# Performance work log

Measured on AMD Instinct MI355X. Metric: run time of the kernel, lower is better.

## Reference

```python
import jax, jax.numpy as jnp
import numpy as np

B, L, D, V = 512, 128, 512, 100000

def setup_inputs() -> dict:
    key = jax.random.key(0)
    ks = jax.random.split(key, 8)
    return {
        "t1s": jax.random.randint(ks[0], (B,), 0, V),
        "t2s": jax.random.randint(ks[1], (B,), 0, V),
        "t1_contexts": jax.random.randint(ks[2], (B, L), 0, V),
        "t2_contexts": jax.random.randint(ks[3], (B, L), 0, V),
        "embed_table": jax.random.normal(ks[4], (V, D), dtype=jnp.float32),
        "att_mat": jax.random.normal(ks[5], (D, D), dtype=jnp.float32) * (6.0 / (D + D)) ** 0.5,
        "w_pred": jax.random.normal(ks[6], (D, 1), dtype=jnp.float32) * 0.02,
        "b_pred": jnp.zeros((1,), dtype=jnp.float32),
    }

def _frob_normalize(x):
    # torch.norm(mat, p=2) is the Frobenius norm of the whole (L, D) matrix
    n = jnp.sqrt(jnp.sum(x * x, axis=(1, 2), keepdims=True))
    return x / n

def reference(t1s, t2s, t1_contexts, t2_contexts, embed_table, att_mat, w_pred, b_pred):
    # dropout is identity in eval mode; t1s/t2s embeddings are unused in the
    # 'dynamic' branch (dead code in the original forward).
    A = _frob_normalize(embed_table[t1_contexts])  # (B, L, D)
    Bm = _frob_normalize(embed_table[t2_contexts])  # (B, L, D)
    # batched bilinear attention: tanh(A @ att_mat @ B^T)
    S = jnp.tanh(jnp.einsum('bld,de,bme->blm', A, att_mat, Bm))  # (B, L, L)
    rows = jax.nn.softmax(jnp.mean(S, axis=2), axis=1)  # (B, L)
    cols = jax.nn.softmax(jnp.mean(S, axis=1), axis=1)  # (B, L)
    newA = jnp.einsum('bld,bl->bd', A, rows)   # (B, D)
    newB = jnp.einsum('bld,bl->bd', Bm, cols)  # (B, D)
    logits = ((newA * newB) @ w_pred + b_pred).reshape(-1)  # (B,)
    return logits, S
```

## Files before the change

### kernel.cpp

```cpp
#include <hip/hip_runtime.h>
#include <hip/hip_bf16.h>
#include <stdint.h>

#define NB 512
#define NL 128
#define ND 512

typedef __bf16 bf16;
typedef __bf16 bf16x8 __attribute__((ext_vector_type(8)));
typedef float  f32x4  __attribute__((ext_vector_type(4)));

#define GLDS(src, dst) __builtin_amdgcn_global_load_lds( \
    (const __attribute__((address_space(1))) void*)(src), \
    (__attribute__((address_space(3))) void*)(dst), 16, 0, 0)

__global__ __launch_bounds__(256) void k_gather(const int* __restrict__ ctx1,
                                                const int* __restrict__ ctx2,
                                                const float* __restrict__ table,
                                                bf16* __restrict__ d1,
                                                bf16* __restrict__ d2,
                                                float* __restrict__ ss,
                                                const float* __restrict__ att,
                                                bf16* __restrict__ attT) {
    const int b = blockIdx.x, side = blockIdx.y, zc = blockIdx.z, t = threadIdx.x;
    if (side == 2) {
        int chunk = b * 8 + zc;
        if (chunk < 1024) {
            int i = chunk * 256 + t;
            int n = i >> 9, k = i & 511;
            attT[i] = (bf16)att[k * 512 + n];
        }
        return;
    }
    const int* __restrict__ ctx = side ? ctx2 : ctx1;
    bf16* __restrict__ dst = side ? d2 : d1;
    const int base = b * NL;
    const int dv = t & 127, lr = t >> 7;
    int idxs[8];
    #pragma unroll
    for (int i = 0; i < 8; ++i) idxs[i] = ctx[base + zc * 16 + i * 2 + lr];
    float acc = 0.f;
    #pragma unroll
    for (int i = 0; i < 8; ++i) {
        int l = zc * 16 + i * 2 + lr;
        f32x4 v = __builtin_nontemporal_load(
            (const f32x4*)table + (size_t)idxs[i] * (ND / 4) + dv);
        acc += v[0]*v[0] + v[1]*v[1] + v[2]*v[2] + v[3]*v[3];
        union { bf16 h[4]; uint2 u; } pk;
        pk.h[0] = (bf16)v[0]; pk.h[1] = (bf16)v[1];
        pk.h[2] = (bf16)v[2]; pk.h[3] = (bf16)v[3];
        *((uint2*)(dst + (size_t)(base + l) * ND) + dv) = pk.u;
    }
    for (int o = 32; o; o >>= 1) acc += __shfl_xor(acc, o);
    __shared__ float red[4];
    if ((t & 63) == 0) red[t >> 6] = acc;
    __syncthreads();
    if (t == 0) atomicAdd(&ss[side * NB + b], red[0] + red[1] + red[2] + red[3]);
}

__global__ __launch_bounds__(512) void k_mega2(
        const bf16* __restrict__ Ab, const bf16* __restrict__ attT,
        const bf16* __restrict__ Bb, float* __restrict__ Sout,
        const float* __restrict__ ss, const float* __restrict__ w_pred,
        const float* __restrict__ b_pred, float* __restrict__ logits) {
    const int b = blockIdx.x, row0 = b * NL, tid = threadIdx.x;
    const int lane = tid & 63, w = tid >> 6;
    const int lm = lane & 15, quad = lane >> 4;
    const int wm  = (w & 1) * 64;
    const int wn1 = (w >> 1) * 128;
    const int wn2 = (w >> 1) * 32;

    __shared__ __align__(16) char smem[163840];
    bf16* stA0 = (bf16*)smem;
    bf16* stA1 = (bf16*)(smem + 8192);
    bf16* stT0 = (bf16*)(smem + 16384);
    bf16* stT1 = (bf16*)(smem + 49152);
    bf16* Tls  = (bf16*)smem;
    bf16* sB0  = (bf16*)(smem + 131072);
    bf16* sB1  = (bf16*)(smem + 139264);
    bf16* sC0  = (bf16*)(smem + 147456);
    bf16* sC1  = (bf16*)(smem + 155648);
    float* rowb = (float*)smem;
    float* colb = (float*)(smem + 2048);
    float* wrow = (float*)(smem + 3072);
    float* wcol = (float*)(smem + 3584);
    float* red2 = (float*)(smem + 4096);

    const float ssA = ss[b], ssB = ss[NB + b];

    #define STAGE1(k0, dA, dT) do {                                          \
        { int r_ = tid >> 2, sl_ = tid & 3, cs_ = sl_ ^ ((r_ >> 1) & 3);     \
          GLDS(Ab + (size_t)(row0 + r_) * ND + (k0) + cs_ * 8, (dA) + tid * 8); } \
        _Pragma("unroll")                                                    \
        for (int i_ = 0; i_ < 4; ++i_) {                                     \
            int s_ = i_ * 512 + tid, r_ = s_ >> 2, sl_ = s_ & 3;             \
            int cs_ = sl_ ^ ((r_ >> 1) & 3);                                 \
            GLDS(attT + (size_t)r_ * ND + (k0) + cs_ * 8, (dT) + s_ * 8); }  \
    } while (0)
    #define STAGE2(k0, dB, dC) do {                                          \
        int r_ = tid >> 2, sl_ = tid & 3, cs_ = sl_ ^ ((r_ >> 1) & 3);       \
        GLDS(Bb + (size_t)(row0 + r_) * ND + (k0) + cs_ * 8, (dB) + tid * 8);\
        GLDS(Ab + (size_t)(row0 + r_) * ND + (k0) + cs_ * 8, (dC) + tid * 8);\
    } while (0)

    f32x4 acc1[4][8] = {};
    STAGE1(0, stA0, stT0);

    for (int t = 0; t < 16; ++t) {
        if (t < 15) {
            STAGE1((t + 1) * 32, (t & 1) ? stA0 : stA1, (t & 1) ? stT0 : stT1);
            asm volatile("s_waitcnt vmcnt(5)" ::: "memory");
        } else {
            STAGE2(0, sB0, sC0);
            asm volatile("s_waitcnt vmcnt(2)" ::: "memory");
        }
        __builtin_amdgcn_s_barrier();
        const bf16* A_ = (t & 1) ? stA1 : stA0;
        const bf16* T_ = (t & 1) ? stT1 : stT0;
        bf16x8 af[4], bfm[8];
        #pragma unroll
        for (int t4 = 0; t4 < 4; ++t4) {
            int R = wm + t4 * 16 + lm;
            af[t4] = *(const bf16x8*)&A_[R * 32 + (quad ^ ((R >> 1) & 3)) * 8];
        }
        #pragma unroll
        for (int t8 = 0; t8 < 8; ++t8) {
            int R = wn1 + t8 * 16 + lm;
            bfm[t8] = *(const bf16x8*)&T_[R * 32 + (quad ^ ((R >> 1) & 3)) * 8];
        }
        __builtin_amdgcn_s_setprio(1);
        #pragma unroll
        for (int im = 0; im < 4; ++im)
            #pragma unroll
            for (int jn = 0; jn < 8; ++jn)
                acc1[im][jn] = __builtin_amdgcn_mfma_f32_16x16x32_bf16(
                    af[im], bfm[jn], acc1[im][jn], 0, 0, 0);
        __builtin_amdgcn_s_setprio(0);
        __builtin_amdgcn_s_barrier();
    }

    #pragma unroll
    for (int im = 0; im < 4; ++im)
    #pragma unroll
    for (int jn = 0; jn < 8; ++jn)
    #pragma unroll
    for (int p = 0; p < 4; ++p) {
        int m = wm + im * 16 + quad * 4 + p;
        int n = wn1 + jn * 16 + lm;
        int ks = n >> 5, kq = (n >> 3) & 3, e = n & 7;
        int pos = kq ^ ((m >> 2) & 3);
        Tls[ks * 4096 + m * 32 + pos * 8 + e] = (bf16)acc1[im][jn][p];
    }
    __syncthreads();

    f32x4 acc2[4][2] = {}, accG[4][2] = {};

    for (int t = 0; t < 16; ++t) {
        if (t < 15) {
            STAGE2((t + 1) * 32, (t & 1) ? sB0 : sB1, (t & 1) ? sC0 : sC1);
            asm volatile("s_waitcnt vmcnt(2)" ::: "memory");
        } else {
            asm volatile("s_waitcnt vmcnt(0)" ::: "memory");
        }
        __builtin_amdgcn_s_barrier();
        const bf16* B_ = (t & 1) ? sB1 : sB0;
        const bf16* C_ = (t & 1) ? sC1 : sC0;
        float4 w0 = *(const float4*)(w_pred + t * 32 + quad * 8);
        float4 w1 = *(const float4*)(w_pred + t * 32 + quad * 8 + 4);
        float wv[8] = {w0.x, w0.y, w0.z, w0.w, w1.x, w1.y, w1.z, w1.w};
        bf16x8 af[4], af2[4], bf2[2], bfw[2];
        #pragma unroll
        for (int t4 = 0; t4 < 4; ++t4) {
            int R = wm + t4 * 16 + lm;
            af[t4]  = *(const bf16x8*)&Tls[t * 4096 + R * 32 + (quad ^ ((R >> 2) & 3)) * 8];
            af2[t4] = *(const bf16x8*)&C_[R * 32 + (quad ^ ((R >> 1) & 3)) * 8];
        }
        #pragma unroll
        for (int t2 = 0; t2 < 2; ++t2) {
            int R = wn2 + t2 * 16 + lm;
            bf2[t2] = *(const bf16x8*)&B_[R * 32 + (quad ^ ((R >> 1) & 3)) * 8];
            #pragma unroll
            for (int j = 0; j < 8; ++j)
                bfw[t2][j] = (bf16)((float)bf2[t2][j] * wv[j]);
        }
        __builtin_amdgcn_s_setprio(1);
        #pragma unroll
        for (int im = 0; im < 4; ++im)
            #pragma unroll
            for (int jn = 0; jn < 2; ++jn) {
                acc2[im][jn] = __builtin_amdgcn_mfma_f32_16x16x32_bf16(
                    af[im], bf2[jn], acc2[im][jn], 0, 0, 0);
                accG[im][jn] = __builtin_amdgcn_mfma_f32_16x16x32_bf16(
                    af2[im], bfw[jn], accG[im][jn], 0, 0, 0);
            }
        __builtin_amdgcn_s_setprio(0);
        __builtin_amdgcn_s_barrier();
    }

    const float sc = rsqrtf(ssA * ssB);
    float* __restrict__ Sb = Sout + (size_t)b * NL * NL;
    #pragma unroll
    for (int im = 0; im < 4; ++im)
    #pragma unroll
    for (int jn = 0; jn < 2; ++jn)
    #pragma unroll
    for (int p = 0; p < 4; ++p) {
        float v = tanhf(acc2[im][jn][p] * sc);
        acc2[im][jn][p] = v;
        int m = wm + im * 16 + quad * 4 + p;
        int n = wn2 + jn * 16 + lm;
        __builtin_nontemporal_store(v, &Sb[m * NL + n]);
    }
    #pragma unroll
    for (int im = 0; im < 4; ++im)
    #pragma unroll
    for (int p = 0; p < 4; ++p) {
        float r = acc2[im][0][p] + acc2[im][1][p];
        r += __shfl_xor(r, 1); r += __shfl_xor(r, 2);
        r += __shfl_xor(r, 4); r += __shfl_xor(r, 8);
        if (lm == 0) rowb[(w >> 1) * NL + wm + im * 16 + quad * 4 + p] = r;
    }
    #pragma unroll
    for (int jn = 0; jn < 2; ++jn) {
        float cv = 0.f;
        #pragma unroll
        for (int im = 0; im < 4; ++im)
            #pragma unroll
            for (int p = 0; p < 4; ++p) cv += acc2[im][jn][p];
        cv += __shfl_xor(cv, 16); cv += __shfl_xor(cv, 32);
        if (quad == 0) colb[(w & 1) * NL + wn2 + jn * 16 + lm] = cv;
    }
    __syncthreads();

    if (tid < 64) {
        float a  = (rowb[tid] + rowb[NL + tid] + rowb[2 * NL + tid] + rowb[3 * NL + tid]) * (1.f / NL);
        float c2 = (rowb[tid + 64] + rowb[NL + tid + 64] + rowb[2 * NL + tid + 64] + rowb[3 * NL + tid + 64]) * (1.f / NL);
        float mx = fmaxf(a, c2);
        for (int o = 32; o; o >>= 1) mx = fmaxf(mx, __shfl_xor(mx, o));
        float e0 = expf(a - mx), e1 = expf(c2 - mx);
        float s = e0 + e1;
        for (int o = 32; o; o >>= 1) s += __shfl_xor(s, o);
        float inv = 1.f / s;
        wrow[tid] = e0 * inv; wrow[tid + 64] = e1 * inv;
    } else if (tid < 128) {
        int q = tid - 64;
        float a  = (colb[q] + colb[NL + q]) * (1.f / NL);
        float c2 = (colb[q + 64] + colb[NL + q + 64]) * (1.f / NL);
        float mx = fmaxf(a, c2);
        for (int o = 32; o; o >>= 1) mx = fmaxf(mx, __shfl_xor(mx, o));
        float e0 = expf(a - mx), e1 = expf(c2 - mx);
        float s = e0 + e1;
        for (int o = 32; o; o >>= 1) s += __shfl_xor(s, o);
        float inv = 1.f / s;
        wcol[q] = e0 * inv; wcol[q + 64] = e1 * inv;
    }
    __syncthreads();

    float wc0 = wcol[wn2 + lm], wc1 = wcol[wn2 + 16 + lm];
    float g = 0.f;
    #pragma unroll
    for (int im = 0; im < 4; ++im)
    #pragma unroll
    for (int p = 0; p < 4; ++p) {
        float wr = wrow[wm + im * 16 + quad * 4 + p];
        g += wr * (wc0 * accG[im][0][p] + wc1 * accG[im][1][p]);
    }
    for (int o = 32; o; o >>= 1) g += __shfl_xor(g, o);
    if (lane == 0) red2[w] = g;
    __syncthreads();
    if (tid == 0) {
        float tot = 0.f;
        #pragma unroll
        for (int i = 0; i < 8; ++i) tot += red2[i];
        logits[b] = tot * sc + b_pred[0];
    }
}

extern "C" void kernel_launch(void* const* d_in, const int* in_sizes, int n_in,
                              void* d_out, int out_size, void* d_ws, size_t ws_size,
                              hipStream_t stream) {
    const int*   t1c = (const int*)d_in[2];
    const int*   t2c = (const int*)d_in[3];
    const float* emb = (const float*)d_in[4];
    const float* att = (const float*)d_in[5];
    const float* wp  = (const float*)d_in[6];
    const float* bp  = (const float*)d_in[7];

    float* out    = (float*)d_out;
    float* logits = out;
    float* S      = out + NB;

    char* ws = (char*)d_ws;
    bf16*  Ab   = (bf16*)(ws);
    bf16*  Bb   = (bf16*)(ws + 67108864);
    bf16*  attT = (bf16*)(ws + 134217728);
    float* ss   = (float*)(ws + 134742016);

    hipMemsetAsync(ss, 0, 4096, stream);
    k_gather<<<dim3(NB, 3, 8), 256, 0, stream>>>(t1c, t2c, emb, Ab, Bb, ss, att, attT);
    k_mega2<<<dim3(NB), 512, 0, stream>>>(Ab, attT, Bb, S, ss, wp, bp, logits);
}
```

Baseline: 398.5 us.

## Move B-side embedding gather into main kernel, overlapped with first GEMM

The second context's embedding gather and sum-of-squares no longer run in the separate gather kernel. They move into the main kernel, where each iteration of the first GEMM loop issues row loads two steps ahead and commits them to the bf16 B buffer. The norm is then reduced in-block, and the B-tile staging now starts after the first phase. This hides the gather's memory latency behind MFMA work and removes half of the gather launch. The cost is more registers and outstanding loads in the main loop, which could lower occupancy or disturb the vmcnt-based pipelining. The B rows are also written to global memory and then read back by the same block, which relies on that ordering being visible.

Measured after the change: 418.6 us. 1.05x slower.

```diff
diff --git a/kernel.cpp b/kernel.cpp
--- a/kernel.cpp
+++ b/kernel.cpp
@@ -15,15 +15,13 @@
     (__attribute__((address_space(3))) void*)(dst), 16, 0, 0)
 
 __global__ __launch_bounds__(256) void k_gather(const int* __restrict__ ctx1,
-                                                const int* __restrict__ ctx2,
                                                 const float* __restrict__ table,
                                                 bf16* __restrict__ d1,
-                                                bf16* __restrict__ d2,
                                                 float* __restrict__ ss,
                                                 const float* __restrict__ att,
                                                 bf16* __restrict__ attT) {
     const int b = blockIdx.x, side = blockIdx.y, zc = blockIdx.z, t = threadIdx.x;
-    if (side == 2) {
+    if (side == 1) {
         int chunk = b * 8 + zc;
         if (chunk < 1024) {
             int i = chunk * 256 + t;
@@ -32,13 +30,11 @@
         }
         return;
     }
-    const int* __restrict__ ctx = side ? ctx2 : ctx1;
-    bf16* __restrict__ dst = side ? d2 : d1;
     const int base = b * NL;
     const int dv = t & 127, lr = t >> 7;
     int idxs[8];
     #pragma unroll
-    for (int i = 0; i < 8; ++i) idxs[i] = ctx[base + zc * 16 + i * 2 + lr];
+    for (int i = 0; i < 8; ++i) idxs[i] = ctx1[base + zc * 16 + i * 2 + lr];
     float acc = 0.f;
     #pragma unroll
     for (int i = 0; i < 8; ++i) {
@@ -49,18 +45,19 @@
         union { bf16 h[4]; uint2 u; } pk;
         pk.h[0] = (bf16)v[0]; pk.h[1] = (bf16)v[1];
         pk.h[2] = (bf16)v[2]; pk.h[3] = (bf16)v[3];
-        *((uint2*)(dst + (size_t)(base + l) * ND) + dv) = pk.u;
+        *((uint2*)(d1 + (size_t)(base + l) * ND) + dv) = pk.u;
     }
     for (int o = 32; o; o >>= 1) acc += __shfl_xor(acc, o);
     __shared__ float red[4];
     if ((t & 63) == 0) red[t >> 6] = acc;
     __syncthreads();
-    if (t == 0) atomicAdd(&ss[side * NB + b], red[0] + red[1] + red[2] + red[3]);
+    if (t == 0) atomicAdd(&ss[b], red[0] + red[1] + red[2] + red[3]);
 }
 
-__global__ __launch_bounds__(512) void k_mega2(
+__global__ __launch_bounds__(512) void k_mega2b(
         const bf16* __restrict__ Ab, const bf16* __restrict__ attT,
-        const bf16* __restrict__ Bb, float* __restrict__ Sout,
+        bf16* __restrict__ Bb, const int* __restrict__ ctx2,
+        const float* __restrict__ table, float* __restrict__ Sout,
         const float* __restrict__ ss, const float* __restrict__ w_pred,
         const float* __restrict__ b_pred, float* __restrict__ logits) {
     const int b = blockIdx.x, row0 = b * NL, tid = threadIdx.x;
@@ -75,6 +72,7 @@
     bf16* stA1 = (bf16*)(smem + 8192);
     bf16* stT0 = (bf16*)(smem + 16384);
     bf16* stT1 = (bf16*)(smem + 49152);
+    float* redB = (float*)(smem + 81920);
     bf16* Tls  = (bf16*)smem;
     bf16* sB0  = (bf16*)(smem + 131072);
     bf16* sB1  = (bf16*)(smem + 139264);
@@ -86,7 +84,29 @@
     float* wcol = (float*)(smem + 3584);
     float* red2 = (float*)(smem + 4096);
 
-    const float ssA = ss[b], ssB = ss[NB + b];
+    const int r8b = w, c8b = lane;
+    int bidx[16];
+    #pragma unroll
+    for (int c = 0; c < 16; ++c) bidx[c] = ctx2[row0 + c * 8 + r8b];
+    const float ssA = ss[b];
+    float pb = 0.f;
+    f32x4 bgl[2][2];
+
+    #define BG_ISSUE(c) do {                                                  \
+        const f32x4* rp_ = (const f32x4*)table + (size_t)bidx[c] * (ND/4) + c8b*2; \
+        bgl[(c)&1][0] = __builtin_nontemporal_load(rp_);                      \
+        bgl[(c)&1][1] = __builtin_nontemporal_load(rp_ + 1);                  \
+    } while (0)
+    #define BG_COMMIT(c) do {                                                 \
+        f32x4 v0_ = bgl[(c)&1][0], v1_ = bgl[(c)&1][1];                       \
+        pb += v0_[0]*v0_[0] + v0_[1]*v0_[1] + v0_[2]*v0_[2] + v0_[3]*v0_[3]   \
+            + v1_[0]*v1_[0] + v1_[1]*v1_[1] + v1_[2]*v1_[2] + v1_[3]*v1_[3];  \
+        union { bf16 h[8]; uint4 u; } pk_;                                    \
+        pk_.h[0]=(bf16)v0_[0]; pk_.h[1]=(bf16)v0_[1]; pk_.h[2]=(bf16)v0_[2];  \
+        pk_.h[3]=(bf16)v0_[3]; pk_.h[4]=(bf16)v1_[0]; pk_.h[5]=(bf16)v1_[1];  \
+        pk_.h[6]=(bf16)v1_[2]; pk_.h[7]=(bf16)v1_[3];                         \
+        *(uint4*)(Bb + (size_t)(row0 + (c)*8 + r8b) * ND + c8b*8) = pk_.u;    \
+    } while (0)
 
     #define STAGE1(k0, dA, dT) do {                                          \
         { int r_ = tid >> 2, sl_ = tid & 3, cs_ = sl_ ^ ((r_ >> 1) & 3);     \
@@ -105,14 +125,16 @@
 
     f32x4 acc1[4][8] = {};
     STAGE1(0, stA0, stT0);
-
+    BG_ISSUE(0); BG_ISSUE(1);
+
+    #pragma unroll
     for (int t = 0; t < 16; ++t) {
+        BG_COMMIT(t);
         if (t < 15) {
             STAGE1((t + 1) * 32, (t & 1) ? stA0 : stA1, (t & 1) ? stT0 : stT1);
-            asm volatile("s_waitcnt vmcnt(5)" ::: "memory");
+            asm volatile("s_waitcnt vmcnt(8)" ::: "memory");
         } else {
-            STAGE2(0, sB0, sC0);
-            asm volatile("s_waitcnt vmcnt(2)" ::: "memory");
+            asm volatile("s_waitcnt vmcnt(1)" ::: "memory");
         }
         __builtin_amdgcn_s_barrier();
         const bf16* A_ = (t & 1) ? stA1 : stA0;
@@ -136,8 +158,16 @@
                 acc1[im][jn] = __builtin_amdgcn_mfma_f32_16x16x32_bf16(
                     af[im], bfm[jn], acc1[im][jn], 0, 0, 0);
         __builtin_amdgcn_s_setprio(0);
+        if (t < 14) BG_ISSUE(t + 2);
         __builtin_amdgcn_s_barrier();
     }
+
+    for (int o = 32; o; o >>= 1) pb += __shfl_xor(pb, o);
+    if (lane == 0) redB[w] = pb;
+    __syncthreads();
+    float ssB = redB[0] + redB[1] + redB[2] + redB[3]
+              + redB[4] + redB[5] + redB[6] + redB[7];
+    __syncthreads();
 
     #pragma unroll
     for (int im = 0; im < 4; ++im)
@@ -154,7 +184,9 @@
     __syncthreads();
 
     f32x4 acc2[4][2] = {}, accG[4][2] = {};
-
+    STAGE2(0, sB0, sC0);
+
+    #pragma unroll
     for (int t = 0; t < 16; ++t) {
         if (t < 15) {
             STAGE2((t + 1) * 32, (t & 1) ? sB0 : sB1, (t & 1) ? sC0 : sC1);
@@ -297,6 +329,7 @@
     float* ss   = (float*)(ws + 134742016);
 
     hipMemsetAsync(ss, 0, 4096, stream);
-    k_gather<<<dim3(NB, 3, 8), 256, 0, stream>>>(t1c, t2c, emb, Ab, Bb, ss, att, attT);
-    k_mega2<<<dim3(NB), 512, 0, stream>>>(Ab, attT, Bb, S, ss, wp, bp, logits);
+    k_gather<<<dim3(NB, 2, 8), 256, 0, stream>>>(t1c, emb, Ab, ss, att, attT);
+    k_mega2b<<<dim3(NB), 512, 0, stream>>>(Ab, attT, Bb, t2c, emb,
+                                           S, ss, wp, bp, logits);
 }
```
